# Optimization experiments

Measured on AMD Instinct MI355X. Metric: run time of the kernel, lower is better.

Reference implementation:

```python
import jax, jax.numpy as jnp
import numpy as np

NUM_PROJS = 7
BLOCK = 32

def _gray_perm(n):
    # unit-hamming-distance (Gray-code) permutation used by AngularLSH
    a = np.array([0, 1], dtype=np.int32)
    for s in range(2, n + 1):
        a = np.concatenate([a, a[::-1] + 2 ** (s - 1)])
    return a

PERM = jnp.asarray(_gray_perm(NUM_PROJS))
ENC = jnp.asarray(2 ** np.arange(NUM_PROJS), dtype=np.int32)  # [R]


def lsh_hash(x, proj_dir):
    # x: [B,H,S,D], proj_dir: [D,R] -> integer bucket ids [B,H,S]
    bits = (jnp.einsum('bhsd,dr->bhsr', x, proj_dir) > 0).astype(jnp.int32)
    code = (bits * ENC).sum(-1)
    return PERM[code]


def sdpa(q, k, v, mask):
    # q,k,v: [...,S,D]; mask: bool broadcastable to [...,Sq,Sk]
    scale = q.shape[-1] ** -0.5
    scores = jnp.einsum('...qd,...kd->...qk', q, k) * scale
    scores = jnp.where(mask, scores, -jnp.inf)
    return jnp.einsum('...qk,...kd->...qd', jax.nn.softmax(scores, axis=-1), v)


def setup_inputs() -> dict:
    key = jax.random.key(0)
    kq, kk, kv, kp = jax.random.split(key, 4)
    B, H, S, D = 2, 16, 2048, 128
    return {
        'q': jax.random.normal(kq, (B, H, S, D), dtype=jnp.float32),
        'k': jax.random.normal(kk, (B, H, S, D), dtype=jnp.float32),
        'v': jax.random.normal(kv, (B, H, S, D), dtype=jnp.float32),
        'proj_dir': jax.random.normal(kp, (D, NUM_PROJS), dtype=jnp.float32),
        'mask': jnp.ones((1, 1, 1, 1), dtype=bool),
    }


def reference(q, k, v, proj_dir, mask):
    B, H, S, D = q.shape
    # 1) LSH hash queries, stable sort along seq dim, reorder queries
    q_hash = lsh_hash(q, proj_dir)                                   # [B,H,S]
    sort_idx = jnp.argsort(q_hash, axis=2, stable=True)              # [B,H,S]
    q_hash_sorted = jnp.take_along_axis(q_hash, sort_idx, axis=2)
    q_sorted = jnp.take_along_axis(q, sort_idx[..., None], axis=2)   # [B,H,S,D]
    # 2) hash keys (unsorted), split into blocks of size BLOCK
    k_hash = lsh_hash(k, proj_dir)                                   # [B,H,S]
    k_hash_blk = k_hash.reshape(-1, 1, BLOCK)                        # [NB,1,32]
    q_hash_blk = q_hash_sorted.reshape(-1, 1, BLOCK)
    # 3) criticality: per-block count of matching hash ids; critical blocks get K zeroed
    criticality = (k_hash_blk == q_hash_blk).sum(-1).squeeze(-1)     # [NB]
    keep = (criticality <= 0).astype(q.dtype)                        # 0 where critical (matches torch loop)
    Qb = q_sorted.reshape(-1, 1, BLOCK, D)                           # [NB,1,32,D]
    Kb = k.reshape(-1, 1, BLOCK, D) * keep[:, None, None, None]
    Vb = v.reshape(-1, 1, BLOCK, D)
    # 4) dual SDPA: blocked critical attention + full dense attention
    out_critical = sdpa(Qb, Kb, Vb, mask).reshape(B, H, S, D)
    out_actual = sdpa(q, k, v, mask)                                 # [B,H,S,D]
    loss = jnp.mean((out_critical - out_actual) ** 2)
    return out_actual, loss
```

## Files before the change

kernel.cpp:

```cpp
#include <hip/hip_runtime.h>
#include <hip/hip_bf16.h>

#define SEQ 2048
#define DIM 128
#define NBH 32
#define NROWS (NBH*SEQ)
#define NBLK (NROWS/32)
#define SCALE 0.08838834764831845f
#define QSC (0.08838834764831845f * 1.4426950408889634f)

typedef __attribute__((ext_vector_type(8))) short short8;
typedef __attribute__((ext_vector_type(16))) float float16;

__device__ __forceinline__ unsigned short f2bf(float x) {
    union { float f; unsigned u; } v; v.f = x;
    unsigned r = v.u + 0x7fffu + ((v.u >> 16) & 1u);
    return (unsigned short)(r >> 16);
}
__device__ __forceinline__ unsigned pack_bf16(float a, float b) {
    float2 f; f.x = a; f.y = b;
    __hip_bfloat162 h = __float22bfloat162_rn(f);
    union { __hip_bfloat162 h2; unsigned u; } cv; cv.h2 = h; return cv.u;
}
__device__ __forceinline__ void gl_lds16(const void* g, void* l) {
    __builtin_amdgcn_global_load_lds((const __attribute__((address_space(1))) unsigned int*)g,
                                     (__attribute__((address_space(3))) unsigned int*)l, 16, 0, 0);
}

__global__ __launch_bounds__(256) void hash_kernel(const float* __restrict__ qg, const float* __restrict__ kg,
                            const float* __restrict__ proj,
                            int* __restrict__ qh, int* __restrict__ kh)
{
    const int gw   = (int)((blockIdx.x * blockDim.x + threadIdx.x) >> 6);
    const int lane = threadIdx.x & 63;
    const int sub  = lane >> 4;
    const int dl   = (lane & 15) * 8;
    const int r    = gw * 4 + sub;
    const float* src; int* dst; int row;
    if (r < NROWS) { src = qg; dst = qh; row = r; }
    else           { src = kg; dst = kh; row = r - NROWS; }

    const float* x = src + (size_t)row * DIM + dl;
    float xv[8];
    {
        float4 f0 = *(const float4*)x;
        float4 f1 = *(const float4*)(x + 4);
        xv[0]=f0.x; xv[1]=f0.y; xv[2]=f0.z; xv[3]=f0.w;
        xv[4]=f1.x; xv[5]=f1.y; xv[6]=f1.z; xv[7]=f1.w;
    }
    float pj[56];
    #pragma unroll
    for (int i = 0; i < 14; ++i)
        *(float4*)&pj[i*4] = *(const float4*)(proj + dl*7 + i*4);

    float a[7] = {0.f,0.f,0.f,0.f,0.f,0.f,0.f};
    #pragma unroll
    for (int d = 0; d < 8; ++d)
        #pragma unroll
        for (int p = 0; p < 7; ++p) a[p] = fmaf(xv[d], pj[d*7+p], a[p]);

    #pragma unroll
    for (int off = 1; off < 16; off <<= 1)
        #pragma unroll
        for (int p = 0; p < 7; ++p) a[p] += __shfl_xor(a[p], off, 64);

    if ((lane & 15) == 0) {
        int code = 0;
        if (a[0] > 0.f) code |= 1;  if (a[1] > 0.f) code |= 2;
        if (a[2] > 0.f) code |= 4;  if (a[3] > 0.f) code |= 8;
        if (a[4] > 0.f) code |= 16; if (a[5] > 0.f) code |= 32;
        if (a[6] > 0.f) code |= 64;
        dst[row] = code ^ (code >> 1);
    }
}

__global__ __launch_bounds__(256) void sort_kernel(const int* __restrict__ qh,
                                                   int* __restrict__ sidx, int* __restrict__ qhs)
{
    __shared__ __align__(16) unsigned short cnt[128][260];
    __shared__ int startv[128];
    const int bh = blockIdx.x;
    const int t  = threadIdx.x;
    const int base = bh*SEQ;

    {
        const short8 z8 = {0,0,0,0,0,0,0,0};
        for (int i = t; i < 4160; i += 256) ((short8*)cnt)[i] = z8;
    }
    __syncthreads();

    int hv[8];
    {
        int4 a = *(const int4*)(qh + base + t*8);
        int4 b = *(const int4*)(qh + base + t*8 + 4);
        hv[0]=a.x; hv[1]=a.y; hv[2]=a.z; hv[3]=a.w;
        hv[4]=b.x; hv[5]=b.y; hv[6]=b.z; hv[7]=b.w;
    }
    #pragma unroll
    for (int i = 0; i < 8; ++i) cnt[hv[i]][t]++;
    __syncthreads();

    const int wv = t >> 6, l = t & 63;
    #pragma unroll 1
    for (int v = wv; v < 128; v += 4) {
        ushort4 cc = *(const ushort4*)&cnt[v][4*l];
        unsigned c0 = cc.x, c1 = cc.y, c2 = cc.z, c3 = cc.w;
        unsigned s01 = c0 + c1;
        unsigned s = s01 + c2 + c3;
        unsigned inc = s;
        #pragma unroll
        for (int off = 1; off < 64; off <<= 1) {
            unsigned o = __shfl_up(inc, off, 64);
            if (l >= off) inc += o;
        }
        unsigned ex = inc - s;
        ushort4 wb;
        wb.x = (unsigned short)ex;
        wb.y = (unsigned short)(ex + c0);
        wb.z = (unsigned short)(ex + s01);
        wb.w = (unsigned short)(ex + s01 + c2);
        *(ushort4*)&cnt[v][4*l] = wb;
        if (l == 63) cnt[v][256] = (unsigned short)inc;
    }
    __syncthreads();

    if (t < 64) {
        int a0 = cnt[2*t][256], a1 = cnt[2*t+1][256];
        int s2 = a0 + a1, inc = s2;
        #pragma unroll
        for (int off = 1; off < 64; off <<= 1) {
            int o = __shfl_up(inc, off, 64);
            if (t >= off) inc += o;
        }
        int ex = inc - s2;
        startv[2*t]   = ex;
        startv[2*t+1] = ex + a0;
    }
    __syncthreads();

    #pragma unroll
    for (int i = 0; i < 8; ++i) {
        const int v = hv[i];
        int prior = 0;
        #pragma unroll
        for (int j = 0; j < 8; ++j) if (j < i && hv[j] == v) ++prior;
        const int rank = startv[v] + (int)cnt[v][t] + prior;
        sidx[base + rank] = t*8 + i;
        qhs[base + rank]  = v;
    }
}

__global__ __launch_bounds__(256) void prep_kernel(const float* __restrict__ kg,
                                                   const float* __restrict__ vg,
                                                   unsigned short* __restrict__ kbf,
                                                   unsigned short* __restrict__ vtg)
{
    __shared__ unsigned short T[128][72];
    const int t  = threadIdx.x;
    const int h  = blockIdx.x >> 5;
    const int sl = blockIdx.x & 31;
    const size_t base = ((size_t)h*SEQ + sl*64) * DIM;

    #pragma unroll
    for (int i = 0; i < 8; ++i) {
        const float4 f = *(const float4*)(kg + base + ((size_t)i*256 + t)*4);
        uint2 pk; pk.x = pack_bf16(f.x, f.y); pk.y = pack_bf16(f.z, f.w);
        *(uint2*)(kbf + base + ((size_t)i*256 + t)*4) = pk;
    }

    const int kk = t & 63, seg = t >> 6;
    #pragma unroll
    for (int i = 0; i < 8; ++i) {
        float4 f = *(const float4*)(vg + base + (size_t)kk*DIM + seg*32 + i*4);
        T[seg*32 + i*4 + 0][kk] = f2bf(f.x);
        T[seg*32 + i*4 + 1][kk] = f2bf(f.y);
        T[seg*32 + i*4 + 2][kk] = f2bf(f.z);
        T[seg*32 + i*4 + 3][kk] = f2bf(f.w);
    }
    __syncthreads();
    const int r = t >> 1, hf = t & 1;
    unsigned short* dst = vtg + ((size_t)h*DIM + r)*SEQ + sl*64 + hf*32;
    #pragma unroll
    for (int i = 0; i < 4; ++i)
        *(short8*)(dst + i*8) = *(const short8*)&T[r][hf*32 + i*8];
}

__global__ __launch_bounds__(256, 2) void dense_attn_mfma(
    const unsigned short* __restrict__ kbf, const unsigned short* __restrict__ vtg,
    const float* __restrict__ qg, float* __restrict__ outg)
{
    __shared__ __align__(16) unsigned short KbF[2*8192];
    __shared__ __align__(16) unsigned short VbF[2*8192];

    const int t    = threadIdx.x;
    const int lane = t & 63;
    const int w    = t >> 6;
    const int q5   = lane >> 5;
    const int l31  = lane & 31;
    const int e    = l31 & 7;

    const int b    = blockIdx.x;
    const int slot = b >> 3;
    const int head = (b & 7) * 4 + (slot >> 4);
    const int qblk = slot & 15;

    const float* Qg = qg + ((size_t)head*SEQ + qblk*128 + w*32) * DIM;
    const unsigned short* Kh = kbf + (size_t)head*SEQ*DIM;
    const unsigned short* Vh = vtg + (size_t)head*DIM*SEQ;

    int koff[8], voff[4];
    #pragma unroll
    for (int ch = 0; ch < 8; ++ch) koff[ch] = l31*128 + (((2*ch + q5) ^ e) * 8);
    #pragma unroll
    for (int u = 0; u < 4; ++u)    voff[u]  = l31*64  + ((((u>>1)*4 + (u&1)*2 + q5) ^ e) * 8);

    const unsigned short* kgp[4]; unsigned short* kls[4];
    const unsigned short* vgp[4]; unsigned short* vls[4];
    #pragma unroll
    for (int i = 0; i < 4; ++i) {
        const int j = w*4 + i;
        const int r = j*4 + (lane >> 4);
        const int u = (lane & 15) ^ (r & 7);
        kgp[i] = Kh + r*DIM + u*8;
        kls[i] = KbF + j*512;
        const int d = j*8 + (lane >> 3);
        const int u2 = (lane & 7) ^ (d & 7);
        vgp[i] = Vh + (size_t)d*SEQ + u2*8;
        vls[i] = VbF + j*512;
    }

    union FR { unsigned u[4]; short8 s; };
    short8 Qf[8];
    #pragma unroll
    for (int ch = 0; ch < 8; ++ch) {
        const float* p = Qg + (size_t)l31*DIM + ch*16 + q5*8;
        float4 f0 = *(const float4*)p;
        float4 f1 = *(const float4*)(p + 4);
        FR fr;
        fr.u[0] = pack_bf16(f0.x*QSC, f0.y*QSC);
        fr.u[1] = pack_bf16(f0.z*QSC, f0.w*QSC);
        fr.u[2] = pack_bf16(f1.x*QSC, f1.y*QSC);
        fr.u[3] = pack_bf16(f1.z*QSC, f1.w*QSC);
        Qf[ch] = fr.s;
    }

    float16 o[4];
    #pragma unroll
    for (int mt = 0; mt < 4; ++mt)
        #pragma unroll
        for (int r = 0; r < 16; ++r) o[mt][r] = 0.f;
    float lsum = 0.f;

    auto stage = [&](const int buf) {
        #pragma unroll
        for (int i = 0; i < 4; ++i) gl_lds16(kgp[i], kls[i] + buf*8192);
        #pragma unroll
        for (int i = 0; i < 4; ++i) gl_lds16(vgp[i], vls[i] + buf*8192);
        #pragma unroll
        for (int i = 0; i < 4; ++i) { kgp[i] += 8192; vgp[i] += 64; }
    };

    auto body = [&](const int buf) {
        #pragma unroll
        for (int s = 0; s < 2; ++s) {
            float16 sv;
            #pragma unroll
            for (int r = 0; r < 16; ++r) sv[r] = 0.f;
            __builtin_amdgcn_s_setprio(1);
            #pragma unroll
            for (int ch = 0; ch < 8; ++ch) {
                short8 kf = *(const short8*)&KbF[buf*8192 + s*4096 + koff[ch]];
                sv = __builtin_amdgcn_mfma_f32_32x32x16_bf16(kf, Qf[ch], sv, 0, 0, 0);
            }
            __builtin_amdgcn_s_setprio(0);
            unsigned pk[8];
            #pragma unroll
            for (int rp = 0; rp < 8; ++rp) {
                float p0 = __builtin_amdgcn_exp2f(sv[2*rp]);
                float p1 = __builtin_amdgcn_exp2f(sv[2*rp+1]);
                lsum += p0 + p1;
                pk[rp] = pack_bf16(p0, p1);
            }
            unsigned e0 = __shfl_xor(q5 ? pk[0] : pk[2], 32, 64);
            unsigned e1 = __shfl_xor(q5 ? pk[1] : pk[3], 32, 64);
            unsigned e2 = __shfl_xor(q5 ? pk[4] : pk[6], 32, 64);
            unsigned e3 = __shfl_xor(q5 ? pk[5] : pk[7], 32, 64);
            FR c0, c1;
            if (q5 == 0) {
                c0.u[0]=pk[0]; c0.u[1]=pk[1]; c0.u[2]=e0;    c0.u[3]=e1;
                c1.u[0]=pk[4]; c1.u[1]=pk[5]; c1.u[2]=e2;    c1.u[3]=e3;
            } else {
                c0.u[0]=e0;    c0.u[1]=e1;    c0.u[2]=pk[2]; c0.u[3]=pk[3];
                c1.u[0]=e2;    c1.u[1]=e3;    c1.u[2]=pk[6]; c1.u[3]=pk[7];
            }
            __builtin_amdgcn_s_setprio(1);
            #pragma unroll
            for (int c = 0; c < 2; ++c) {
                short8 pf = c ? c1.s : c0.s;
                #pragma unroll
                for (int mt = 0; mt < 4; ++mt) {
                    short8 vf = *(const short8*)&VbF[buf*8192 + mt*2048 + voff[s*2 + c]];
                    o[mt] = __builtin_amdgcn_mfma_f32_32x32x16_bf16(vf, pf, o[mt], 0, 0, 0);
                }
            }
            __builtin_amdgcn_s_setprio(0);
        }
    };

    stage(0);
    #pragma unroll 1
    for (int kt2 = 0; kt2 < 16; ++kt2) {
        __syncthreads();
        stage(1);
        body(0);
        __syncthreads();
        if (kt2 < 15) stage(0);
        body(1);
    }

    const float l = lsum + __shfl_xor(lsum, 32, 64);
    const float inv = 1.f / l;
    float* orow = outg + ((size_t)head*SEQ + qblk*128 + w*32 + l31) * DIM;
    #pragma unroll
    for (int mt = 0; mt < 4; ++mt)
        #pragma unroll
        for (int rg = 0; rg < 4; ++rg) {
            const int d0 = mt*32 + rg*8 + q5*4;
            float4 ov;
            ov.x = o[mt][rg*4+0]*inv; ov.y = o[mt][rg*4+1]*inv;
            ov.z = o[mt][rg*4+2]*inv; ov.w = o[mt][rg*4+3]*inv;
            *(float4*)(orow + d0) = ov;
        }
}

__global__ __launch_bounds__(256) void crit_attn(
    const unsigned short* __restrict__ kbf, const unsigned short* __restrict__ vtg,
    const float* __restrict__ qg, const int* __restrict__ sidx,
    const int* __restrict__ kh, const int* __restrict__ qhs,
    const float* __restrict__ outg, float* __restrict__ lossp)
{
    __shared__ float wsum[4];
    const int t    = threadIdx.x;
    const int lane = t & 63;
    const int w    = t >> 6;
    const int nb   = blockIdx.x * 4 + w;
    const int q5   = lane >> 5;
    const int l31  = lane & 31;
    const int bh   = nb >> 6;

    const int khv = kh[nb*32 + l31];
    const int qhv = qhs[nb*32 + l31];
    const unsigned long long mm = __ballot(khv == qhv);
    const float kp = ((mm & 0xffffffffull) == 0ull) ? 1.0f : 0.0f;

    const int qrow = sidx[bh*SEQ + (nb & 63)*32 + l31];

    union FR { unsigned u[4]; short8 s; };
    short8 Qf[8];
    const float* Qg = qg + ((size_t)bh*SEQ + qrow) * DIM;
    #pragma unroll
    for (int ch = 0; ch < 8; ++ch) {
        const float* p = Qg + ch*16 + q5*8;
        float4 f0 = *(const float4*)p;
        float4 f1 = *(const float4*)(p + 4);
        FR fr;
        fr.u[0] = pack_bf16(f0.x*QSC, f0.y*QSC);
        fr.u[1] = pack_bf16(f0.z*QSC, f0.w*QSC);
        fr.u[2] = pack_bf16(f1.x*QSC, f1.y*QSC);
        fr.u[3] = pack_bf16(f1.z*QSC, f1.w*QSC);
        Qf[ch] = fr.s;
    }

    const unsigned short* Kb = kbf + (size_t)(nb*32) * DIM;
    float16 sv, sw;
    #pragma unroll
    for (int r = 0; r < 16; ++r) { sv[r] = 0.f; sw[r] = 0.f; }
    #pragma unroll
    for (int ch = 0; ch < 4; ++ch) {
        short8 kf = *(const short8*)(Kb + (size_t)l31*DIM + ch*16 + q5*8);
        sv = __builtin_amdgcn_mfma_f32_32x32x16_bf16(kf, Qf[ch], sv, 0, 0, 0);
        short8 kg2 = *(const short8*)(Kb + (size_t)l31*DIM + (ch+4)*16 + q5*8);
        sw = __builtin_amdgcn_mfma_f32_32x32x16_bf16(kg2, Qf[ch+4], sw, 0, 0, 0);
    }

    float lsum = 0.f;
    unsigned pk[8];
    #pragma unroll
    for (int rp = 0; rp < 8; ++rp) {
        float p0 = __builtin_amdgcn_exp2f((sv[2*rp]   + sw[2*rp])   * kp);
        float p1 = __builtin_amdgcn_exp2f((sv[2*rp+1] + sw[2*rp+1]) * kp);
        lsum += p0 + p1;
        pk[rp] = pack_bf16(p0, p1);
    }
    unsigned e0 = __shfl_xor(q5 ? pk[0] : pk[2], 32, 64);
    unsigned e1 = __shfl_xor(q5 ? pk[1] : pk[3], 32, 64);
    unsigned e2 = __shfl_xor(q5 ? pk[4] : pk[6], 32, 64);
    unsigned e3 = __shfl_xor(q5 ? pk[5] : pk[7], 32, 64);
    FR c0, c1;
    if (q5 == 0) {
        c0.u[0]=pk[0]; c0.u[1]=pk[1]; c0.u[2]=e0;    c0.u[3]=e1;
        c1.u[0]=pk[4]; c1.u[1]=pk[5]; c1.u[2]=e2;    c1.u[3]=e3;
    } else {
        c0.u[0]=e0;    c0.u[1]=e1;    c0.u[2]=pk[2]; c0.u[3]=pk[3];
        c1.u[0]=e2;    c1.u[1]=e3;    c1.u[2]=pk[6]; c1.u[3]=pk[7];
    }
    const float ltot = lsum + __shfl_xor(lsum, 32, 64);

    const unsigned short* Vb = vtg + (size_t)bh*DIM*SEQ + (size_t)(nb & 63)*32;
    float16 o[4];
    #pragma unroll
    for (int mt = 0; mt < 4; ++mt)
        #pragma unroll
        for (int r = 0; r < 16; ++r) o[mt][r] = 0.f;
    #pragma unroll
    for (int c = 0; c < 2; ++c) {
        short8 pf = c ? c1.s : c0.s;
        #pragma unroll
        for (int mt = 0; mt < 4; ++mt) {
            short8 vf = *(const short8*)(Vb + (size_t)(mt*32 + l31)*SEQ + c*16 + q5*8);
            o[mt] = __builtin_amdgcn_mfma_f32_32x32x16_bf16(vf, pf, o[mt], 0, 0, 0);
        }
    }

    const float inv = 1.f / ltot;
    const float* oa_row = outg + (size_t)(nb*32 + l31) * DIM;
    float sq = 0.f;
    #pragma unroll
    for (int mt = 0; mt < 4; ++mt)
        #pragma unroll
        for (int rg = 0; rg < 4; ++rg) {
            const int d0 = mt*32 + rg*8 + q5*4;
            float4 oa = *(const float4*)(oa_row + d0);
            float dx = o[mt][rg*4+0]*inv - oa.x;
            float dy = o[mt][rg*4+1]*inv - oa.y;
            float dz = o[mt][rg*4+2]*inv - oa.z;
            float dw = o[mt][rg*4+3]*inv - oa.w;
            sq += dx*dx + dy*dy + dz*dz + dw*dw;
        }
    #pragma unroll
    for (int off = 32; off > 0; off >>= 1) sq += __shfl_down(sq, off, 64);
    if (lane == 0) wsum[w] = sq;
    __syncthreads();
    if (t == 0) atomicAdd(lossp, (wsum[0]+wsum[1]+wsum[2]+wsum[3]) * (1.0f/8388608.0f));
}

extern "C" void kernel_launch(void* const* d_in, const int* in_sizes, int n_in,
                              void* d_out, int out_size, void* d_ws, size_t ws_size,
                              hipStream_t stream)
{
    const float* q    = (const float*)d_in[0];
    const float* k    = (const float*)d_in[1];
    const float* v    = (const float*)d_in[2];
    const float* proj = (const float*)d_in[3];
    float* out   = (float*)d_out;
    float* lossp = out + (out_size - 1);

    int* qh   = (int*)d_ws;
    int* kh   = qh + NROWS;
    int* sidx = kh + NROWS;
    int* qhs  = sidx + NROWS;
    unsigned short* kbf = (unsigned short*)(qhs + NROWS);
    unsigned short* vtg = kbf + (size_t)NROWS*DIM;

    hipMemsetAsync(lossp, 0, sizeof(float), stream);
    prep_kernel<<<NBH*32, 256, 0, stream>>>(k, v, kbf, vtg);
    hash_kernel<<<(2*NROWS)/16, 256, 0, stream>>>(q, k, proj, qh, kh);
    sort_kernel<<<NBH, 256, 0, stream>>>(qh, sidx, qhs);
    dense_attn_mfma<<<512, 256, 0, stream>>>(kbf, vtg, q, out);
    crit_attn<<<NBLK/4, 256, 0, stream>>>(kbf, vtg, q, sidx, kh, qhs, out, lossp);
}
```

Measured before the change: 278.8 us.

## Fuse critical-block attention and loss into dense attention kernel epilogue

```diff
diff --git a/kernel.cpp b/kernel.cpp
--- a/kernel.cpp
+++ b/kernel.cpp
@@ -187,10 +187,13 @@
 
 __global__ __launch_bounds__(256, 2) void dense_attn_mfma(
     const unsigned short* __restrict__ kbf, const unsigned short* __restrict__ vtg,
-    const float* __restrict__ qg, float* __restrict__ outg)
+    const float* __restrict__ qg, float* __restrict__ outg,
+    const int* __restrict__ sidx, const int* __restrict__ kh,
+    const int* __restrict__ qhs, float* __restrict__ lossp)
 {
     __shared__ __align__(16) unsigned short KbF[2*8192];
     __shared__ __align__(16) unsigned short VbF[2*8192];
+    __shared__ float wsum[4];
 
     const int t    = threadIdx.x;
     const int lane = t & 63;
@@ -266,13 +269,11 @@
             float16 sv;
             #pragma unroll
             for (int r = 0; r < 16; ++r) sv[r] = 0.f;
-            __builtin_amdgcn_s_setprio(1);
             #pragma unroll
             for (int ch = 0; ch < 8; ++ch) {
                 short8 kf = *(const short8*)&KbF[buf*8192 + s*4096 + koff[ch]];
                 sv = __builtin_amdgcn_mfma_f32_32x32x16_bf16(kf, Qf[ch], sv, 0, 0, 0);
             }
-            __builtin_amdgcn_s_setprio(0);
             unsigned pk[8];
             #pragma unroll
             for (int rp = 0; rp < 8; ++rp) {
@@ -293,7 +294,6 @@
                 c0.u[0]=e0;    c0.u[1]=e1;    c0.u[2]=pk[2]; c0.u[3]=pk[3];
                 c1.u[0]=e2;    c1.u[1]=e3;    c1.u[2]=pk[6]; c1.u[3]=pk[7];
             }
-            __builtin_amdgcn_s_setprio(1);
             #pragma unroll
             for (int c = 0; c < 2; ++c) {
                 short8 pf = c ? c1.s : c0.s;
@@ -303,7 +303,6 @@
                     o[mt] = __builtin_amdgcn_mfma_f32_32x32x16_bf16(vf, pf, o[mt], 0, 0, 0);
                 }
             }
-            __builtin_amdgcn_s_setprio(0);
         }
     };
 
@@ -331,36 +330,21 @@
             ov.z = o[mt][rg*4+2]*inv; ov.w = o[mt][rg*4+3]*inv;
             *(float4*)(orow + d0) = ov;
         }
-}
-
-__global__ __launch_bounds__(256) void crit_attn(
-    const unsigned short* __restrict__ kbf, const unsigned short* __restrict__ vtg,
-    const float* __restrict__ qg, const int* __restrict__ sidx,
-    const int* __restrict__ kh, const int* __restrict__ qhs,
-    const float* __restrict__ outg, float* __restrict__ lossp)
-{
-    __shared__ float wsum[4];
-    const int t    = threadIdx.x;
-    const int lane = t & 63;
-    const int w    = t >> 6;
-    const int nb   = blockIdx.x * 4 + w;
-    const int q5   = lane >> 5;
-    const int l31  = lane & 31;
-    const int bh   = nb >> 6;
+
+    const int nb = head*64 + qblk*4 + w;
 
     const int khv = kh[nb*32 + l31];
     const int qhv = qhs[nb*32 + l31];
     const unsigned long long mm = __ballot(khv == qhv);
     const float kp = ((mm & 0xffffffffull) == 0ull) ? 1.0f : 0.0f;
 
-    const int qrow = sidx[bh*SEQ + (nb & 63)*32 + l31];
-
-    union FR { unsigned u[4]; short8 s; };
-    short8 Qf[8];
-    const float* Qg = qg + ((size_t)bh*SEQ + qrow) * DIM;
+    const int qrow = sidx[head*SEQ + (qblk*4 + w)*32 + l31];
+
+    short8 Qf2[8];
+    const float* Qg2 = qg + ((size_t)head*SEQ + qrow) * DIM;
     #pragma unroll
     for (int ch = 0; ch < 8; ++ch) {
-        const float* p = Qg + ch*16 + q5*8;
+        const float* p = Qg2 + ch*16 + q5*8;
         float4 f0 = *(const float4*)p;
         float4 f1 = *(const float4*)(p + 4);
         FR fr;
@@ -368,7 +352,7 @@
         fr.u[1] = pack_bf16(f0.z*QSC, f0.w*QSC);
         fr.u[2] = pack_bf16(f1.x*QSC, f1.y*QSC);
         fr.u[3] = pack_bf16(f1.z*QSC, f1.w*QSC);
-        Qf[ch] = fr.s;
+        Qf2[ch] = fr.s;
     }
 
     const unsigned short* Kb = kbf + (size_t)(nb*32) * DIM;
@@ -378,65 +362,54 @@
     #pragma unroll
     for (int ch = 0; ch < 4; ++ch) {
         short8 kf = *(const short8*)(Kb + (size_t)l31*DIM + ch*16 + q5*8);
-        sv = __builtin_amdgcn_mfma_f32_32x32x16_bf16(kf, Qf[ch], sv, 0, 0, 0);
+        sv = __builtin_amdgcn_mfma_f32_32x32x16_bf16(kf, Qf2[ch], sv, 0, 0, 0);
         short8 kg2 = *(const short8*)(Kb + (size_t)l31*DIM + (ch+4)*16 + q5*8);
-        sw = __builtin_amdgcn_mfma_f32_32x32x16_bf16(kg2, Qf[ch+4], sw, 0, 0, 0);
-    }
-
-    float lsum = 0.f;
-    unsigned pk[8];
+        sw = __builtin_amdgcn_mfma_f32_32x32x16_bf16(kg2, Qf2[ch+4], sw, 0, 0, 0);
+    }
+
+    float lsum2 = 0.f;
+    unsigned pk2[8];
     #pragma unroll
     for (int rp = 0; rp < 8; ++rp) {
         float p0 = __builtin_amdgcn_exp2f((sv[2*rp]   + sw[2*rp])   * kp);
         float p1 = __builtin_amdgcn_exp2f((sv[2*rp+1] + sw[2*rp+1]) * kp);
-        lsum += p0 + p1;
-        pk[rp] = pack_bf16(p0, p1);
-    }
-    unsigned e0 = __shfl_xor(q5 ? pk[0] : pk[2], 32, 64);
-    unsigned e1 = __shfl_xor(q5 ? pk[1] : pk[3], 32, 64);
-    unsigned e2 = __shfl_xor(q5 ? pk[4] : pk[6], 32, 64);
-    unsigned e3 = __shfl_xor(q5 ? pk[5] : pk[7], 32, 64);
-    FR c0, c1;
+        lsum2 += p0 + p1;
+        pk2[rp] = pack_bf16(p0, p1);
+    }
+    unsigned f0 = __shfl_xor(q5 ? pk2[0] : pk2[2], 32, 64);
+    unsigned f1 = __shfl_xor(q5 ? pk2[1] : pk2[3], 32, 64);
+    unsigned f2 = __shfl_xor(q5 ? pk2[4] : pk2[6], 32, 64);
+    unsigned f3 = __shfl_xor(q5 ? pk2[5] : pk2[7], 32, 64);
+    FR d0c, d1c;
     if (q5 == 0) {
-        c0.u[0]=pk[0]; c0.u[1]=pk[1]; c0.u[2]=e0;    c0.u[3]=e1;
-        c1.u[0]=pk[4]; c1.u[1]=pk[5]; c1.u[2]=e2;    c1.u[3]=e3;
+        d0c.u[0]=pk2[0]; d0c.u[1]=pk2[1]; d0c.u[2]=f0;     d0c.u[3]=f1;
+        d1c.u[0]=pk2[4]; d1c.u[1]=pk2[5]; d1c.u[2]=f2;     d1c.u[3]=f3;
     } else {
-        c0.u[0]=e0;    c0.u[1]=e1;    c0.u[2]=pk[2]; c0.u[3]=pk[3];
-        c1.u[0]=e2;    c1.u[1]=e3;    c1.u[2]=pk[6]; c1.u[3]=pk[7];
-    }
-    const float ltot = lsum + __shfl_xor(lsum, 32, 64);
-
-    const unsigned short* Vb = vtg + (size_t)bh*DIM*SEQ + (size_t)(nb & 63)*32;
-    float16 o[4];
-    #pragma unroll
-    for (int mt = 0; mt < 4; ++mt)
-        #pragma unroll
-        for (int r = 0; r < 16; ++r) o[mt][r] = 0.f;
-    #pragma unroll
-    for (int c = 0; c < 2; ++c) {
-        short8 pf = c ? c1.s : c0.s;
-        #pragma unroll
-        for (int mt = 0; mt < 4; ++mt) {
+        d0c.u[0]=f0;     d0c.u[1]=f1;     d0c.u[2]=pk2[2]; d0c.u[3]=pk2[3];
+        d1c.u[0]=f2;     d1c.u[1]=f3;     d1c.u[2]=pk2[6]; d1c.u[3]=pk2[7];
+    }
+    const float ltot2 = lsum2 + __shfl_xor(lsum2, 32, 64);
+    const float inv2  = 1.f / ltot2;
+
+    const unsigned short* Vb = vtg + (size_t)head*DIM*SEQ + (size_t)(qblk*4 + w)*32;
+    float sq = 0.f;
+    #pragma unroll
+    for (int mt = 0; mt < 4; ++mt) {
+        float16 o2;
+        #pragma unroll
+        for (int r = 0; r < 16; ++r) o2[r] = 0.f;
+        #pragma unroll
+        for (int c = 0; c < 2; ++c) {
+            short8 pf = c ? d1c.s : d0c.s;
             short8 vf = *(const short8*)(Vb + (size_t)(mt*32 + l31)*SEQ + c*16 + q5*8);
-            o[mt] = __builtin_amdgcn_mfma_f32_32x32x16_bf16(vf, pf, o[mt], 0, 0, 0);
-        }
-    }
-
-    const float inv = 1.f / ltot;
-    const float* oa_row = outg + (size_t)(nb*32 + l31) * DIM;
-    float sq = 0.f;
-    #pragma unroll
-    for (int mt = 0; mt < 4; ++mt)
-        #pragma unroll
-        for (int rg = 0; rg < 4; ++rg) {
-            const int d0 = mt*32 + rg*8 + q5*4;
-            float4 oa = *(const float4*)(oa_row + d0);
-            float dx = o[mt][rg*4+0]*inv - oa.x;
-            float dy = o[mt][rg*4+1]*inv - oa.y;
-            float dz = o[mt][rg*4+2]*inv - oa.z;
-            float dw = o[mt][rg*4+3]*inv - oa.w;
-            sq += dx*dx + dy*dy + dz*dz + dw*dw;
-        }
+            o2 = __builtin_amdgcn_mfma_f32_32x32x16_bf16(vf, pf, o2, 0, 0, 0);
+        }
+        #pragma unroll
+        for (int r = 0; r < 16; ++r) {
+            float d = o2[r]*inv2 - o[mt][r]*inv;
+            sq += d*d;
+        }
+    }
     #pragma unroll
     for (int off = 32; off > 0; off >>= 1) sq += __shfl_down(sq, off, 64);
     if (lane == 0) wsum[w] = sq;
@@ -466,6 +439,5 @@
     prep_kernel<<<NBH*32, 256, 0, stream>>>(k, v, kbf, vtg);
     hash_kernel<<<(2*NROWS)/16, 256, 0, stream>>>(q, k, proj, qh, kh);
     sort_kernel<<<NBH, 256, 0, stream>>>(qh, sidx, qhs);
-    dense_attn_mfma<<<512, 256, 0, stream>>>(kbf, vtg, q, out);
-    crit_attn<<<NBLK/4, 256, 0, stream>>>(kbf, vtg, q, sidx, kh, qhs, out, lossp);
-}
+    dense_attn_mfma<<<512, 256, 0, stream>>>(kbf, vtg, q, out, sidx, kh, qhs, lossp);
+}
```

New measurement: 263.3 us. 5.6% less time.
